# Performance work log

Measured on AMD Instinct MI355X. Metric: run time of the kernel, lower is better.

Reference implementation:

```python
import jax, jax.numpy as jnp
import numpy as np

B, LQ, E = 4, 8400, 256
HEADS, LEVELS, POINTS = 8, 4, 4
HEAD_DIM = E // HEADS
SHAPES = [(80, 80), (40, 40), (20, 20), (10, 10)]  # (H, W) per level; sum HW = 8400
LV = sum(h * w for h, w in SHAPES)


def setup_inputs() -> dict:
    key = jax.random.key(0)
    ks = jax.random.split(key, 12)
    query = jax.random.normal(ks[0], (B, LQ, E), jnp.float32)
    # per-level normalized reference points in (0.1, 0.9)
    reference_points = 0.1 + 0.8 * jax.random.uniform(ks[1], (B, LQ, LEVELS, 2), jnp.float32)
    value = jax.random.normal(ks[2], (B, LV, E), jnp.float32)
    spatial_shapes = jnp.array(SHAPES, dtype=jnp.int32)
    s = 0.05
    Wv = jax.random.normal(ks[3], (E, E), jnp.float32) * s
    bv = jnp.zeros((E,), jnp.float32)
    Woff = jax.random.normal(ks[4], (E, HEADS * LEVELS * POINTS * 2), jnp.float32) * 0.01
    boff = jax.random.normal(ks[5], (HEADS * LEVELS * POINTS * 2,), jnp.float32) * 0.02
    Wattn = jax.random.normal(ks[6], (E, HEADS * LEVELS * POINTS), jnp.float32) * s
    battn = jnp.zeros((HEADS * LEVELS * POINTS,), jnp.float32)
    Wo = jax.random.normal(ks[7], (E, E), jnp.float32) * s
    bo = jnp.zeros((E,), jnp.float32)
    return dict(query=query, reference_points=reference_points, value=value,
                spatial_shapes=spatial_shapes, Wv=Wv, bv=bv, Woff=Woff, boff=boff,
                Wattn=Wattn, battn=battn, Wo=Wo, bo=bo)


def _bilinear_sample(vflat, x, y, Hl, Wl):
    # vflat: [BH, D, Hl*Wl]; x, y: [BH, N] pixel coords (align_corners=False convention)
    x0f = jnp.floor(x); y0f = jnp.floor(y)
    wx = (x - x0f)[:, None, :]; wy = (y - y0f)[:, None, :]
    x0 = x0f.astype(jnp.int32); y0 = y0f.astype(jnp.int32)

    def gather(ix, iy):
        valid = ((ix >= 0) & (ix < Wl) & (iy >= 0) & (iy < Hl)).astype(vflat.dtype)
        idx = jnp.clip(iy, 0, Hl - 1) * Wl + jnp.clip(ix, 0, Wl - 1)
        g = jnp.take_along_axis(vflat, idx[:, None, :], axis=2)  # [BH, D, N]
        return g * valid[:, None, :]

    v00 = gather(x0, y0); v01 = gather(x0 + 1, y0)
    v10 = gather(x0, y0 + 1); v11 = gather(x0 + 1, y0 + 1)
    return (v00 * (1 - wx) * (1 - wy) + v01 * wx * (1 - wy)
            + v10 * (1 - wx) * wy + v11 * wx * wy)


def _msda_forward(query, reference_points, value, spatial_shapes,
                  Wv, bv, Woff, boff, Wattn, battn, Wo, bo):
    b, lq, _ = query.shape
    v = (value @ Wv + bv).reshape(b, -1, HEADS, HEAD_DIM)
    off = (query @ Woff + boff).reshape(b, lq, HEADS, LEVELS, POINTS, 2)
    aw = (query @ Wattn + battn).reshape(b, lq, HEADS, LEVELS * POINTS)
    aw = jax.nn.softmax(aw, axis=-1).reshape(b, lq, HEADS, LEVELS, POINTS)
    # normalizer (W, H) per level
    norm = jnp.stack([spatial_shapes[:, 1], spatial_shapes[:, 0]], axis=-1).astype(query.dtype)
    # sampling locations in [0,1]: [B, Lq, H, L, P, 2]
    loc = reference_points[:, :, None, :, None, :] + off / norm[None, None, None, :, None, :]

    sampled_levels = []
    start = 0
    for lvl, (Hl, Wl) in enumerate(SHAPES):
        vl = v[:, start:start + Hl * Wl]                      # [B, Hl*Wl, H, D]
        start += Hl * Wl
        vflat = vl.transpose(0, 2, 3, 1).reshape(b * HEADS, HEAD_DIM, Hl * Wl)
        grid = loc[:, :, :, lvl]                              # [B, Lq, H, P, 2]
        grid = grid.transpose(0, 2, 1, 3, 4).reshape(b * HEADS, lq * POINTS, 2)
        g = grid * 2.0 - 1.0                                  # grid_sample convention
        x = (g[..., 0] + 1.0) * (Wl * 0.5) - 0.5
        y = (g[..., 1] + 1.0) * (Hl * 0.5) - 0.5
        s = _bilinear_sample(vflat, x, y, Hl, Wl)             # [BH, D, Lq*P]
        sampled_levels.append(s.reshape(b, HEADS, HEAD_DIM, lq, POINTS))
    sampled = jnp.stack(sampled_levels, axis=-1)              # [B, H, D, Lq, P, L]
    out = jnp.einsum('bhdqpl,bqhlp->bqhd', sampled, aw).reshape(b, lq, E)
    return out @ Wo + bo


def reference(query, reference_points, value, spatial_shapes,
              Wv, bv, Woff, boff, Wattn, battn, Wo, bo):
    return _msda_forward(query, reference_points, value, spatial_shapes,
                         Wv, bv, Woff, boff, Wattn, battn, Wo, bo)
```

## Files before the change

kernel.cpp:

```cpp
#include <hip/hip_runtime.h>
#include <math.h>

#define BB 4
#define LQ 8400
#define NH 8
#define LVTOT 8500
#define HD 32
#define PLANE_USH 544000

typedef __attribute__((ext_vector_type(8))) short short8;
typedef __attribute__((ext_vector_type(4))) float f32x4;
typedef __attribute__((ext_vector_type(2))) _Float16 half2_t;
typedef __attribute__((ext_vector_type(2))) __fp16 fp16x2_t;
typedef unsigned short ushort_t;

__device__ __forceinline__ ushort_t f2bf(float f) {
    union { float f; unsigned u; } v; v.f = f;
    unsigned r = v.u + 0x7fffu + ((v.u >> 16) & 1u);
    return (ushort_t)(r >> 16);
}
__device__ __forceinline__ float bflo(unsigned u) {
    union { unsigned u; float f; } x; x.u = u << 16; return x.f;
}
__device__ __forceinline__ float bfhi(unsigned u) {
    union { unsigned u; float f; } x; x.u = u & 0xffff0000u; return x.f;
}
__device__ __forceinline__ half2_t ash2(unsigned u) {
    union { unsigned u; half2_t h; } x; x.u = u; return x.h;
}
__device__ __forceinline__ unsigned pk2u(fp16x2_t h) {
    union { fp16x2_t h; unsigned u; } x; x.h = h; return x.u;
}

__device__ __forceinline__ void dma16(const ushort_t* g, ushort_t* l) {
    __builtin_amdgcn_global_load_lds(
        (const __attribute__((address_space(1))) void*)g,
        (__attribute__((address_space(3))) void*)l, 16, 0, 0);
}

__global__ __launch_bounds__(256) void prep_all(
    const float* __restrict__ value, const float* __restrict__ query,
    const float* __restrict__ Wv, const float* __restrict__ Woff,
    const float* __restrict__ Wattn, const float* __restrict__ Wo,
    ushort_t* __restrict__ value_b, ushort_t* __restrict__ query_b,
    ushort_t* __restrict__ BT)
{
    const int bid = blockIdx.x;
    if (bid < 16900) {
        const float* src = (bid < 8500) ? value : query;
        ushort_t* dst = (bid < 8500) ? value_b : query_b;
        int i = (bid < 8500 ? bid : bid - 8500) * 256 + threadIdx.x;
        float4 f = ((const float4*)src)[i];
        ushort4 o;
        o.x = f2bf(f.x); o.y = f2bf(f.y); o.z = f2bf(f.z); o.w = f2bf(f.w);
        ((ushort4*)dst)[i] = o;
    } else {
        int idx = (bid - 16900) * 256 + threadIdx.x;
        int r = idx >> 8, k = idx & 255;
        float v;
        if (r < 256) v = Wv[k * 256 + r];
        else if (r < 640) {
            int n = r - 256;
            v = (n < 256) ? Woff[k * 256 + n] : Wattn[k * 128 + (n - 256)];
        } else v = Wo[k * 256 + (r - 640)];
        BT[idx] = f2bf(v);
    }
}

__device__ __forceinline__ void gemm_core(
    const ushort_t* __restrict__ A, const ushort_t* __restrict__ B, int M,
    int m0, int n0, ushort_t* Asl, ushort_t* Bsl, f32x4 acc[4][4])
{
    const int tid  = threadIdx.x;
    const int wave = tid >> 6, lane = tid & 63;
    const int quad = lane >> 4, mr = lane & 15;
    const int wm   = (wave >> 1) * 64, wn = (wave & 1) * 64;
    const int oct  = lane >> 3;
    const int bseg = lane & 7;

    for (int k0 = 0; k0 < 256; k0 += 64) {
        __syncthreads();
        #pragma unroll
        for (int i = 0; i < 4; i++) {
            int m  = i * 32 + wave * 8 + oct;
            int gs = bseg ^ (m & 7);
            int am = min(m0 + m, M - 1);
            dma16(A + (size_t)am * 256 + k0 + gs * 8,
                  Asl + (size_t)(i * 32 + wave * 8) * 64 + lane * 8);
            int bn = n0 + m;
            dma16(B + (size_t)bn * 256 + k0 + gs * 8,
                  Bsl + (size_t)(i * 32 + wave * 8) * 64 + lane * 8);
        }
        __syncthreads();
        #pragma unroll
        for (int ks = 0; ks < 2; ks++) {
            short8 af[4], bf[4];
            const int ksl = ks * 4 + quad;
            #pragma unroll
            for (int i = 0; i < 4; i++) {
                int m = wm + i * 16 + mr;
                af[i] = *(const short8*)&Asl[m * 64 + (ksl ^ (m & 7)) * 8];
                int n = wn + i * 16 + mr;
                bf[i] = *(const short8*)&Bsl[n * 64 + (ksl ^ (n & 7)) * 8];
            }
            #pragma unroll
            for (int i = 0; i < 4; i++)
                #pragma unroll
                for (int j = 0; j < 4; j++)
                    acc[i][j] = __builtin_amdgcn_mfma_f32_16x16x32_bf16(
                        af[i], bf[j], acc[i][j], 0, 0, 0);
        }
    }
}

__global__ __launch_bounds__(256, 3) void gemm_fused(
    const ushort_t* __restrict__ Av, const ushort_t* __restrict__ Aq,
    const ushort_t* __restrict__ BT,
    const float* __restrict__ bv, const float* __restrict__ boff,
    const float* __restrict__ battn,
    ushort_t* __restrict__ vperm, ushort_t* __restrict__ off_b,
    ushort_t* __restrict__ awl_b)
{
    __shared__ ushort_t Asl[128 * 64];
    __shared__ ushort_t Bsl[128 * 64];

    const int bid = blockIdx.x;
    int mode, m0, n0, M;
    const ushort_t *A, *B;
    if (bid < 532) { mode = 0; m0 = (bid >> 1) * 128; n0 = (bid & 1) * 128;
                     A = Av; B = BT; M = 34000; }
    else { int b2 = bid - 532;
           mode = 1; m0 = (b2 / 3) * 128; n0 = (b2 % 3) * 128;
           A = Aq; B = BT + 65536; M = 33600; }

    f32x4 acc[4][4];
    #pragma unroll
    for (int i = 0; i < 4; i++)
        #pragma unroll
        for (int j = 0; j < 4; j++) acc[i][j] = (f32x4){0.f, 0.f, 0.f, 0.f};

    gemm_core(A, B, M, m0, n0, Asl, Bsl, acc);

    const int tid  = threadIdx.x;
    const int wave = tid >> 6, lane = tid & 63;
    const int quad = lane >> 4, mr = lane & 15;
    const int wm   = (wave >> 1) * 64, wn = (wave & 1) * 64;

    #pragma unroll
    for (int i = 0; i < 4; i++) {
        const int rbase = m0 + wm + i * 16 + quad * 4;
        #pragma unroll
        for (int j = 0; j < 4; j++) {
            const int c = n0 + wn + j * 16 + mr;
            #pragma unroll
            for (int reg = 0; reg < 4; reg++) {
                int row = rbase + reg;
                if (row >= M) continue;
                float val = acc[i][j][reg];
                if (mode == 0) {
                    float o = val + bv[c];
                    int b = row / LVTOT, pix = row - b * LVTOT;
                    int h = c >> 5, d = c & 31;
                    union { _Float16 h16; ushort_t u; } cv;
                    cv.h16 = (_Float16)o;
                    int lb, y, x, rowp;
                    if (pix < 6400)      { int rel = pix;        y = rel / 80; x = rel - y * 80; rowp = 40; lb = 0; }
                    else if (pix < 8000) { int rel = pix - 6400; y = rel / 40; x = rel - y * 40; rowp = 20; lb = 3200; }
                    else if (pix < 8400) { int rel = pix - 8000; y = rel / 20; x = rel - y * 20; rowp = 10; lb = 4000; }
                    else                 { int rel = pix - 8400; y = rel / 10; x = rel - y * 10; rowp = 5;  lb = 4200; }
                    size_t plane = (size_t)(b * NH + h) * PLANE_USH;
                    int yb = lb + y * rowp;
                    int i0 = (yb + (x >> 1)) * 64 + d * 2 + (x & 1);
                    int p1 = x ? ((x - 1) >> 1) : (rowp - 1);
                    int s1 = x ? ((x - 1) & 1) : 1;
                    int i1 = (4250 + yb + p1) * 64 + d * 2 + s1;
                    vperm[plane + i0] = cv.u;
                    vperm[plane + i1] = cv.u;
                } else {
                    if (c < 256) off_b[(size_t)row * 256 + c] = f2bf(val + boff[c]);
                    else awl_b[(size_t)row * 128 + (c - 256)] = f2bf(val + battn[c - 256]);
                }
            }
        }
    }
}

__global__ __launch_bounds__(256, 3) void gemm_out(
    const ushort_t* __restrict__ A, const ushort_t* __restrict__ BT,
    const float* __restrict__ bo, float* __restrict__ out)
{
    __shared__ ushort_t Asl[128 * 64];
    __shared__ ushort_t Bsl[128 * 64];

    const int m0 = (blockIdx.x >> 1) * 128;
    const int n0 = (blockIdx.x & 1) * 128;
    const int M = 33600;

    f32x4 acc[4][4];
    #pragma unroll
    for (int i = 0; i < 4; i++)
        #pragma unroll
        for (int j = 0; j < 4; j++) acc[i][j] = (f32x4){0.f, 0.f, 0.f, 0.f};

    gemm_core(A, BT, M, m0, n0, Asl, Bsl, acc);

    const int tid  = threadIdx.x;
    const int wave = tid >> 6, lane = tid & 63;
    const int quad = lane >> 4, mr = lane & 15;
    const int wm   = (wave >> 1) * 64, wn = (wave & 1) * 64;

    #pragma unroll
    for (int i = 0; i < 4; i++) {
        const int rbase = m0 + wm + i * 16 + quad * 4;
        #pragma unroll
        for (int j = 0; j < 4; j++) {
            const int c = n0 + wn + j * 16 + mr;
            #pragma unroll
            for (int reg = 0; reg < 4; reg++) {
                int row = rbase + reg;
                if (row >= M) continue;
                out[(size_t)row * 256 + c] = acc[i][j][reg] + bo[c];
            }
        }
    }
}

__global__ __launch_bounds__(256) void msda_sample(
    const ushort_t* __restrict__ vperm, const ushort_t* __restrict__ off,
    const ushort_t* __restrict__ awl, const float* __restrict__ refp,
    ushort_t* __restrict__ sampled)
{
    __shared__ int4 s_wi[16 * 33];

    const int tid = threadIdx.x;
    const int bid = blockIdx.x;
    const int h   = bid & 7;
    const int r   = bid >> 3;
    const int b   = r / 263;
    const int c   = r - b * 263;
    const int q0b = c * 32;
    const size_t bq0 = (size_t)b * LQ + q0b;

    const int Hs[4]    = {80, 40, 20, 10};
    const int pbase[4] = {0, 3200, 4000, 4200};

    #pragma unroll
    for (int it = 0; it < 2; it++) {
        const int s  = it * 256 + tid;
        const int ql = s >> 4, lp = s & 15;
        const int l  = lp >> 2;
        const int qv = (q0b + ql < LQ) ? ql : 0;
        const size_t bq = bq0 + qv;
        const int Wl = Hs[l];

        unsigned od = *(const unsigned*)(off + bq * 256 + h * 32 + lp * 2);
        float ox = bflo(od), oy = bfhi(od);
        float lgt = bflo((unsigned)awl[bq * 128 + h * 16 + lp]);
        float e = __expf(lgt);
        float sum = e;
        sum += __shfl_xor(sum, 1, 16);
        sum += __shfl_xor(sum, 2, 16);
        sum += __shfl_xor(sum, 4, 16);
        sum += __shfl_xor(sum, 8, 16);
        float aw = e * __builtin_amdgcn_rcpf(sum);

        float2 rp = *(const float2*)(refp + bq * 8 + l * 2);
        float x = rp.x * (float)Wl + ox - 0.5f;
        float y = rp.y * (float)Wl + oy - 0.5f;
        float x0f = floorf(x), y0f = floorf(y);
        float wx = x - x0f, wy = y - y0f;
        int x0 = (int)x0f, y0 = (int)y0f;
        float hx0 = ((x0 >= 0) & (x0 < Wl)) ? (1.f - wx) : 0.f;
        float hx1 = ((x0 + 1 >= 0) & (x0 + 1 < Wl)) ? wx : 0.f;
        float vy0w = ((y0 >= 0) & (y0 < Wl)) ? (1.f - wy) * aw : 0.f;
        float vy1w = ((y0 + 1 >= 0) & (y0 + 1 < Wl)) ? wy * aw : 0.f;
        int px = min(max(x0, 0), Wl - 2);
        float pl, pr;
        if (x0 < px)      { pl = hx1; pr = 0.f; }
        else if (x0 > px) { pl = 0.f; pr = hx0; }
        else              { pl = hx0; pr = hx1; }
        int cy0 = min(max(y0, 0), Wl - 1);
        int cy1 = min(max(y0 + 1, 0), Wl - 1);
        const int copy = px & 1;
        const int p    = copy ? ((px - 1) >> 1) : (px >> 1);
        const int rowp = Wl >> 1;
        const int cb   = copy * 4250 + pbase[l] + p;
        const int otop = (cb + cy0 * rowp) << 7;
        const int obot = (cb + cy1 * rowp) << 7;
        unsigned wt = pk2u(__builtin_amdgcn_cvt_pkrtz(pl * vy0w, pr * vy0w));
        unsigned wb = pk2u(__builtin_amdgcn_cvt_pkrtz(pl * vy1w, pr * vy1w));
        s_wi[lp * 33 + ql] = make_int4((int)wt, (int)wb, otop, obot);
    }
    __syncthreads();

    const int ql  = tid >> 3;
    const int l8  = tid & 7;
    const int dby = l8 * 16;

    if (q0b + ql < LQ) {
        const char* plane = (const char*)(vperm + (size_t)(b * NH + h) * PLANE_USH);
        float a0 = 0.f, a1 = 0.f, a2 = 0.f, a3 = 0.f;
        #pragma unroll
        for (int pt = 0; pt < 16; pt++) {
            int4 wi = s_wi[pt * 33 + ql];
            uint4 vt = *(const uint4*)(plane + (unsigned)(wi.z + dby));
            uint4 vb = *(const uint4*)(plane + (unsigned)(wi.w + dby));
            half2_t wt = ash2((unsigned)wi.x);
            half2_t wb = ash2((unsigned)wi.y);
            a0 = __builtin_amdgcn_fdot2(wt, ash2(vt.x), a0, false);
            a0 = __builtin_amdgcn_fdot2(wb, ash2(vb.x), a0, false);
            a1 = __builtin_amdgcn_fdot2(wt, ash2(vt.y), a1, false);
            a1 = __builtin_amdgcn_fdot2(wb, ash2(vb.y), a1, false);
            a2 = __builtin_amdgcn_fdot2(wt, ash2(vt.z), a2, false);
            a2 = __builtin_amdgcn_fdot2(wb, ash2(vb.z), a2, false);
            a3 = __builtin_amdgcn_fdot2(wt, ash2(vt.w), a3, false);
            a3 = __builtin_amdgcn_fdot2(wb, ash2(vb.w), a3, false);
        }
        const size_t bq = bq0 + ql;
        ushort4 o;
        o.x = f2bf(a0); o.y = f2bf(a1);
        o.z = f2bf(a2); o.w = f2bf(a3);
        *(ushort4*)(sampled + bq * 256 + h * 32 + l8 * 4) = o;
    }
}

extern "C" void kernel_launch(void* const* d_in, const int* in_sizes, int n_in,
                              void* d_out, int out_size, void* d_ws, size_t ws_size,
                              hipStream_t stream) {
    const float* query = (const float*)d_in[0];
    const float* refp  = (const float*)d_in[1];
    const float* value = (const float*)d_in[2];
    const float* Wv    = (const float*)d_in[4];
    const float* bv    = (const float*)d_in[5];
    const float* Woff  = (const float*)d_in[6];
    const float* boff  = (const float*)d_in[7];
    const float* Wattn = (const float*)d_in[8];
    const float* battn = (const float*)d_in[9];
    const float* Wo    = (const float*)d_in[10];
    const float* bo    = (const float*)d_in[11];
    float* out = (float*)d_out;

    ushort_t* ws = (ushort_t*)d_ws;
    ushort_t* off_b   = ws;
    ushort_t* awl_b   = off_b + 8601600;
    ushort_t* value_b = awl_b + 4300800;
    ushort_t* query_b = value_b + 8704000;
    ushort_t* vperm_b = query_b + 8601600;
    ushort_t* BT      = vperm_b + 17408000;
    ushort_t* sampled_b = query_b;

    prep_all<<<dim3(17796), 256, 0, stream>>>(
        value, query, Wv, Woff, Wattn, Wo, value_b, query_b, BT);

    gemm_fused<<<dim3(532 + 789), 256, 0, stream>>>(
        value_b, query_b, BT, bv, boff, battn, vperm_b, off_b, awl_b);

    msda_sample<<<dim3(8 * 4 * 263), 256, 0, stream>>>(
        vperm_b, off_b, awl_b, refp, sampled_b);

    gemm_out<<<dim3(526), 256, 0, stream>>>(
        sampled_b, BT + 163840, bo, out);
}
```

Before: 228.0 us.

## Stage GEMM epilogue through swizzled LDS for coalesced vector stores

The fused GEMM epilogue now writes biased, converted results into a swizzled shared-memory tile and then re-reads them to emit 16-byte vector stores. Before, each thread did scattered 2-byte global writes. For the value projection it builds the paired-pixel permuted layout directly from LDS, with special handling for tile-boundary pixels whose partner lives in a neighbouring tile. This aims to cut uncoalesced store traffic, at the cost of extra syncs, LDS reuse and more complex indexing that could hide edge-case bugs.

```diff
diff --git a/kernel.cpp b/kernel.cpp
--- a/kernel.cpp
+++ b/kernel.cpp
@@ -36,6 +36,14 @@
     __builtin_amdgcn_global_load_lds(
         (const __attribute__((address_space(1))) void*)g,
         (__attribute__((address_space(3))) void*)l, 16, 0, 0);
+}
+
+__device__ __forceinline__ void lvl_decomp(int pix, int& lb, int& y, int& x,
+                                           int& rowp) {
+    if (pix < 6400)      { y = pix / 80;            x = pix - y * 80;  rowp = 40; lb = 0; }
+    else if (pix < 8000) { int r = pix - 6400; y = r / 40; x = r - y * 40; rowp = 20; lb = 3200; }
+    else if (pix < 8400) { int r = pix - 8000; y = r / 20; x = r - y * 20; rowp = 10; lb = 4000; }
+    else                 { int r = pix - 8400; y = r / 10; x = r - y * 10; rowp = 5;  lb = 4200; }
 }
 
 __global__ __launch_bounds__(256) void prep_all(
@@ -121,8 +129,9 @@
     ushort_t* __restrict__ vperm, ushort_t* __restrict__ off_b,
     ushort_t* __restrict__ awl_b)
 {
-    __shared__ ushort_t Asl[128 * 64];
-    __shared__ ushort_t Bsl[128 * 64];
+    __shared__ ushort_t smem[16384];
+    ushort_t* Asl = smem;
+    ushort_t* Bsl = smem + 8192;
 
     const int bid = blockIdx.x;
     int mode, m0, n0, M;
@@ -146,39 +155,89 @@
     const int quad = lane >> 4, mr = lane & 15;
     const int wm   = (wave >> 1) * 64, wn = (wave & 1) * 64;
 
+    __syncthreads();
     #pragma unroll
     for (int i = 0; i < 4; i++) {
-        const int rbase = m0 + wm + i * 16 + quad * 4;
         #pragma unroll
         for (int j = 0; j < 4; j++) {
-            const int c = n0 + wn + j * 16 + mr;
+            const int lc = wn + j * 16 + mr;
+            const int c  = n0 + lc;
+            const float bias = (mode == 0) ? bv[c]
+                              : (c < 256 ? boff[c] : battn[c - 256]);
             #pragma unroll
             for (int reg = 0; reg < 4; reg++) {
-                int row = rbase + reg;
-                if (row >= M) continue;
-                float val = acc[i][j][reg];
-                if (mode == 0) {
-                    float o = val + bv[c];
-                    int b = row / LVTOT, pix = row - b * LVTOT;
-                    int h = c >> 5, d = c & 31;
-                    union { _Float16 h16; ushort_t u; } cv;
-                    cv.h16 = (_Float16)o;
-                    int lb, y, x, rowp;
-                    if (pix < 6400)      { int rel = pix;        y = rel / 80; x = rel - y * 80; rowp = 40; lb = 0; }
-                    else if (pix < 8000) { int rel = pix - 6400; y = rel / 40; x = rel - y * 40; rowp = 20; lb = 3200; }
-                    else if (pix < 8400) { int rel = pix - 8000; y = rel / 20; x = rel - y * 20; rowp = 10; lb = 4000; }
-                    else                 { int rel = pix - 8400; y = rel / 10; x = rel - y * 10; rowp = 5;  lb = 4200; }
-                    size_t plane = (size_t)(b * NH + h) * PLANE_USH;
-                    int yb = lb + y * rowp;
-                    int i0 = (yb + (x >> 1)) * 64 + d * 2 + (x & 1);
-                    int p1 = x ? ((x - 1) >> 1) : (rowp - 1);
-                    int s1 = x ? ((x - 1) & 1) : 1;
-                    int i1 = (4250 + yb + p1) * 64 + d * 2 + s1;
-                    vperm[plane + i0] = cv.u;
-                    vperm[plane + i1] = cv.u;
-                } else {
-                    if (c < 256) off_b[(size_t)row * 256 + c] = f2bf(val + boff[c]);
-                    else awl_b[(size_t)row * 128 + (c - 256)] = f2bf(val + battn[c - 256]);
+                const int rl = wm + i * 16 + quad * 4 + reg;
+                float val = acc[i][j][reg] + bias;
+                ushort_t u;
+                if (mode == 0) { union { _Float16 h; ushort_t u; } cv;
+                                 cv.h = (_Float16)val; u = cv.u; }
+                else u = f2bf(val);
+                smem[rl * 128 + (lc ^ ((rl & 3) << 3))] = u;
+            }
+        }
+    }
+    __syncthreads();
+
+    if (mode == 1) {
+        for (int k = 0; k < 8; k++) {
+            int sid = k * 256 + tid;
+            int rl = sid >> 4, cc = (sid & 15) * 8;
+            int row = m0 + rl;
+            if (row >= M) continue;
+            uint4 v = *(const uint4*)&smem[rl * 128 + (cc ^ ((rl & 3) << 3))];
+            if (n0 < 256) *(uint4*)&off_b[(size_t)row * 256 + n0 + cc] = v;
+            else          *(uint4*)&awl_b[(size_t)row * 128 + cc] = v;
+        }
+    } else {
+        const int hb = n0 >> 5;
+        for (int k = 0; k < 16; k++) {
+            int sid = k * 256 + tid;
+            int unit = sid >> 5;
+            if (unit >= 127) continue;
+            int sub = sid & 31;
+            int hh = sub >> 3, q = sub & 7;
+            int copy = (unit >= 64) ? 1 : 0;
+            int t = copy ? ((unit - 64) * 2 + 1) : (unit * 2);
+            int row = m0 + t;
+            if (row + 1 >= 34000) continue;
+            int b = row / LVTOT, pix = row - b * LVTOT;
+            int lb, y, x, rowp;
+            lvl_decomp(pix, lb, y, x, rowp);
+            if (copy && x >= 2 * rowp - 1) continue;
+            int p = x >> 1;
+            int pidx = copy * 4250 + lb + y * rowp + p;
+            int h = hb + hh;
+            uint2 a  = *(const uint2*)&smem[t * 128 +
+                          ((hh * 32 + q * 4) ^ ((t & 3) << 3))];
+            uint2 b2 = *(const uint2*)&smem[(t + 1) * 128 +
+                          ((hh * 32 + q * 4) ^ (((t + 1) & 3) << 3))];
+            uint4 o;
+            o.x = (a.x & 0xffffu) | (b2.x << 16);
+            o.y = (a.x >> 16)     | (b2.x & 0xffff0000u);
+            o.z = (a.y & 0xffffu) | (b2.y << 16);
+            o.w = (a.y >> 16)     | (b2.y & 0xffff0000u);
+            *(uint4*)((char*)(vperm + (size_t)(b * NH + h) * PLANE_USH)
+                      + (size_t)pidx * 128 + q * 16) = o;
+        }
+        {
+            int pixsel = tid >> 7;
+            int rem = tid & 127;
+            int hh = rem >> 5, d = rem & 31;
+            int t = pixsel ? 127 : 0;
+            int row = m0 + t;
+            if (row < 34000) {
+                int b = row / LVTOT, pix = row - b * LVTOT;
+                int lb, y, x, rowp;
+                lvl_decomp(pix, lb, y, x, rowp);
+                bool doit; int p, slot;
+                if (!pixsel) { doit = (x >= 2);            p = (x - 2) >> 1; slot = 1; }
+                else         { doit = (x < 2 * rowp - 1);  p = (x - 1) >> 1; slot = 0; }
+                if (doit) {
+                    int pidx = 4250 + lb + y * rowp + p;
+                    int h = hb + hh;
+                    vperm[(size_t)(b * NH + h) * PLANE_USH
+                          + (size_t)pidx * 64 + d * 2 + slot] =
+                        smem[t * 128 + ((hh * 32 + d) ^ ((t & 3) << 3))];
                 }
             }
         }
```

Result: faster. 217.8 us (-4.5%).
